# Performance work log

Hardware: AMD Instinct MI355X
Metric: run time of the kernel (lower is better)

## Reference

```python
import jax, jax.numpy as jnp
import numpy as np
from jax import lax

B, C, H, W = 32, 512, 32, 32
NH = 8
ER = 4
DK_RATIO = 0.2
EPS_LN = 1e-6


def _layernorm(t, g, b):
    m = t.mean(-1, keepdims=True)
    v = ((t - m) ** 2).mean(-1, keepdims=True)
    return (t - m) / jnp.sqrt(v + EPS_LN) * g + b


def setup_inputs() -> dict:
    key = jax.random.key(0)
    ks = jax.random.split(key, 24)
    s = 0.02
    dh = C // NH
    return {
        "x": jax.random.normal(ks[0], (B, C, H, W), jnp.float32),
        "mask_u": jax.random.uniform(ks[1], (B, NH, dh, dh), jnp.float32),
        "dw_w": jax.random.normal(ks[2], (C, 1, 3, 3), jnp.float32) * s,
        "dw_b": jnp.zeros((C,), jnp.float32),
        "ln1_g": jnp.ones((C,), jnp.float32),
        "ln1_b": jnp.zeros((C,), jnp.float32),
        "qkv_w": jax.random.normal(ks[3], (3 * C, C), jnp.float32) * s,
        "qkv_b": jnp.zeros((3 * C,), jnp.float32),
        "temp": jnp.ones((NH, 1, 1), jnp.float32),
        "proj_w": jax.random.normal(ks[4], (C, C), jnp.float32) * s,
        "proj_b": jnp.zeros((C,), jnp.float32),
        "ct_w": jax.random.normal(ks[5], (C, C, 2, 2), jnp.float32) * s,  # [in,out,kH,kW]
        "ct_b": jnp.zeros((C,), jnp.float32),
        "ln2_g": jnp.ones((C,), jnp.float32),
        "ln2_b": jnp.zeros((C,), jnp.float32),
        "pw1_w": jax.random.normal(ks[6], (ER * C, C), jnp.float32) * s,
        "pw1_b": jnp.zeros((ER * C,), jnp.float32),
        "pw2_w": jax.random.normal(ks[7], (C, ER * C), jnp.float32) * s,
        "pw2_b": jnp.zeros((C,), jnp.float32),
    }


def reference(x, mask_u, dw_w, dw_b, ln1_g, ln1_b, qkv_w, qkv_b, temp,
              proj_w, proj_b, ct_w, ct_b, ln2_g, ln2_b,
              pw1_w, pw1_b, pw2_w, pw2_b):
    inp = x
    b, c, h, w = x.shape
    # depthwise 3x3 conv + residual
    dw = lax.conv_general_dilated(
        x, dw_w, (1, 1), "SAME", feature_group_count=c,
        dimension_numbers=("NCHW", "OIHW", "NCHW")) + dw_b[None, :, None, None]
    x = dw + inp
    # 2x2 avg pool, stride 2
    hp, wp = h // 2, w // 2
    x = x.reshape(b, c, hp, 2, wp, 2).mean(axis=(3, 5))  # [B,C,hp,wp]
    n = hp * wp
    # tokens [B,N,C] -> LN -> qkv
    t = x.reshape(b, c, n).transpose(0, 2, 1)
    t = _layernorm(t, ln1_g, ln1_b)
    qkv = t @ qkv_w.T + qkv_b                       # [B,N,3C]
    dh = c // NH
    qkv = qkv.reshape(b, n, 3, NH, dh).transpose(2, 0, 3, 1, 4)  # [3,B,h,N,d]
    # cosine (XCA-style) attention: transpose to [B,h,d,N], normalize over N
    q = jnp.swapaxes(qkv[0], -2, -1)
    k = jnp.swapaxes(qkv[1], -2, -1)
    v = jnp.swapaxes(qkv[2], -2, -1)
    q = q / jnp.maximum(jnp.linalg.norm(q, axis=-1, keepdims=True), 1e-12)
    k = k / jnp.maximum(jnp.linalg.norm(k, axis=-1, keepdims=True), 1e-12)
    attn = jnp.einsum("bhdn,bhen->bhde", q, k) * temp  # [B,h,d,d]
    attn = attn + (mask_u < DK_RATIO).astype(attn.dtype) * (-1e12)
    attn = jax.nn.softmax(attn, axis=-1)
    out = jnp.einsum("bhde,bhen->bhdn", attn, v)       # [B,h,d,N]
    out = out.transpose(0, 3, 1, 2).reshape(b, n, c)
    t = out @ proj_w.T + proj_b
    t = t + t
    x = t.transpose(0, 2, 1).reshape(b, c, hp, wp)
    # ConvTranspose2d(C,C,2,stride=2): each pixel expands to 2x2 block
    x = jnp.einsum("bchw,copq->bohpwq", x, ct_w).reshape(b, c, 2 * hp, 2 * wp)
    x = x + ct_b[None, :, None, None]
    # MLP in channels-last
    y = x.transpose(0, 2, 3, 1)                        # [B,H,W,C]
    y = _layernorm(y, ln2_g, ln2_b)
    y = jax.nn.gelu(y @ pw1_w.T + pw1_b, approximate=False)
    y = y @ pw2_w.T + pw2_b
    x = y.transpose(0, 3, 1, 2)
    return inp + x
```

## Files before the change

kernel.cpp:

```cpp
#include <hip/hip_runtime.h>
#include <hip/hip_bf16.h>
#include <math.h>

typedef unsigned short ushort;
typedef __attribute__((ext_vector_type(8))) short short8;
typedef __attribute__((ext_vector_type(8))) unsigned short ushort8;
typedef __attribute__((ext_vector_type(4))) unsigned short ushort4v;
typedef __attribute__((ext_vector_type(4))) float f32x4;

__device__ __forceinline__ ushort f2bb(float v) {
    return __builtin_bit_cast(ushort, __float2bfloat16(v));
}
__device__ __forceinline__ float bf2f(ushort u) {
    return __bfloat162float(__builtin_bit_cast(__hip_bfloat16, u));
}
__device__ __forceinline__ void gl2lds16(const ushort* g, ushort* l) {
    __builtin_amdgcn_global_load_lds(
        (const __attribute__((address_space(1))) unsigned int*)g,
        (__attribute__((address_space(3))) unsigned int*)l, 16, 0, 0);
}


__global__ __launch_bounds__(256) void cvtw_k(const float* __restrict__ in,
                                              ushort* __restrict__ out, int n4) {
    int i = blockIdx.x * 256 + threadIdx.x;
    if (i >= n4) return;
    float4 v = ((const float4*)in)[i];
    ushort4v o;
    o.x = f2bb(v.x); o.y = f2bb(v.y); o.z = f2bb(v.z); o.w = f2bb(v.w);
    ((ushort4v*)out)[i] = o;
}

__global__ __launch_bounds__(256) void cvtt_k(const float* __restrict__ in,
                                              ushort* __restrict__ out) {
    __shared__ float tl[32][33];
    int c0 = blockIdx.y * 32, j0 = blockIdx.x * 32;
    int tr = threadIdx.x >> 5, tc = threadIdx.x & 31;
#pragma unroll
    for (int p4 = 0; p4 < 4; ++p4)
        tl[tr + p4 * 8][tc] = in[(size_t)(c0 + tr + p4 * 8) * 2048 + j0 + tc];
    __syncthreads();
#pragma unroll
    for (int p4 = 0; p4 < 4; ++p4)
        out[(size_t)(j0 + tr + p4 * 8) * 512 + c0 + tc] = f2bb(tl[tc][tr + p4 * 8]);
}

__global__ __launch_bounds__(256) void dwpool_k(const float* __restrict__ x,
                                                const float* __restrict__ dww,
                                                const float* __restrict__ dwb,
                                                ushort* __restrict__ xp) {
    int bc = blockIdx.x;
    int c = bc & 511;
    __shared__ float tile[32][33];
    __shared__ float w9[9];
    const float* xb = x + (size_t)bc * 1024;
    int tid = threadIdx.x;
    for (int i = tid; i < 1024; i += 256) tile[i >> 5][i & 31] = xb[i];
    if (tid < 9) w9[tid] = dww[c * 9 + tid];
    __syncthreads();
    float bv = dwb[c];
    int ph = tid >> 4, pw = tid & 15;
    float s = 0.f;
#pragma unroll
    for (int dy = 0; dy < 2; ++dy) {
#pragma unroll
        for (int dx = 0; dx < 2; ++dx) {
            int hh = 2 * ph + dy, ww = 2 * pw + dx;
            float a = bv + tile[hh][ww];
#pragma unroll
            for (int ky = 0; ky < 3; ++ky) {
                int yy = hh + ky - 1;
                if (yy < 0 || yy > 31) continue;
#pragma unroll
                for (int kx = 0; kx < 3; ++kx) {
                    int xx = ww + kx - 1;
                    if (xx < 0 || xx > 31) continue;
                    a += w9[ky * 3 + kx] * tile[yy][xx];
                }
            }
            s += a;
        }
    }
    xp[(size_t)bc * 256 + tid] = f2bb(0.25f * s);
}

__global__ __launch_bounds__(256) void ln1_stats_k(const ushort* __restrict__ xp,
                                                   float* __restrict__ m1,
                                                   float* __restrict__ r1) {
    __shared__ float sh_s[4][64], sh_q[4][64];
    int blk = blockIdx.x;
    int b = blk >> 2;
    int n0 = (blk & 3) * 64;
    int t = threadIdx.x & 63, w = threadIdx.x >> 6;
    float s = 0.f, ss = 0.f;
    for (int i = 0; i < 128; ++i) {
        int c = w * 128 + i;
        float v = bf2f(xp[(size_t)(b * 512 + c) * 256 + n0 + t]);
        s += v; ss += v * v;
    }
    sh_s[w][t] = s; sh_q[w][t] = ss;
    __syncthreads();
    if (w == 0) {
        s  = sh_s[0][t] + sh_s[1][t] + sh_s[2][t] + sh_s[3][t];
        ss = sh_q[0][t] + sh_q[1][t] + sh_q[2][t] + sh_q[3][t];
        float m = s * (1.0f / 512.0f);
        m1[b * 256 + n0 + t] = m;
        r1[b * 256 + n0 + t] = rsqrtf(ss * (1.0f / 512.0f) - m * m + 1e-6f);
    }
}

__global__ __launch_bounds__(256) void ln1_apply_k(const ushort* __restrict__ xp,
                                                   const float* __restrict__ m1,
                                                   const float* __restrict__ r1,
                                                   const float* __restrict__ g,
                                                   const float* __restrict__ beta,
                                                   ushort* __restrict__ a_ln) {
    __shared__ float tl[64][66];
    int blk = blockIdx.x;
    int b = blk >> 5, ct = (blk >> 2) & 7, nt = blk & 3;
    int t = threadIdx.x;
    int rq = t >> 6, nl = t & 63;
#pragma unroll
    for (int i = 0; i < 16; ++i) {
        int r = rq * 16 + i;
        int c = ct * 64 + r;
        tl[r][nl] = bf2f(xp[(size_t)(b * 512 + c) * 256 + nt * 64 + nl]);
    }
    __syncthreads();
    int r2 = t >> 2, cq = t & 3;
    int m = b * 256 + nt * 64 + r2;
    float mu = m1[m], rs = r1[m];
#pragma unroll
    for (int hh = 0; hh < 2; ++hh) {
        ushort8 o;
#pragma unroll
        for (int j = 0; j < 8; ++j) {
            int cl = cq * 16 + hh * 8 + j;
            int c = ct * 64 + cl;
            o[j] = f2bb((tl[cl][r2] - mu) * rs * g[c] + beta[c]);
        }
        *(ushort8*)&a_ln[(size_t)m * 512 + ct * 64 + cq * 16 + hh * 8] = o;
    }
}

__global__ __launch_bounds__(256) void ln2_fuse_k(ushort* __restrict__ yB,
                                                  ushort* __restrict__ yT,
                                                  const float* __restrict__ g,
                                                  const float* __restrict__ beta) {
    int w = threadIdx.x >> 6, lane = threadIdx.x & 63;
    int row = blockIdx.x * 4 + w;
    ushort* base = (row < 8192) ? (yB + (size_t)row * 512)
                                : (yT + (size_t)(row - 8192) * 512);
    ushort8 raw = *(ushort8*)&base[lane * 8];
    float v[8];
    float s = 0.f, ss = 0.f;
#pragma unroll
    for (int j = 0; j < 8; ++j) { v[j] = bf2f(raw[j]); s += v[j]; ss += v[j] * v[j]; }
#pragma unroll
    for (int off = 1; off < 64; off <<= 1) { s += __shfl_xor(s, off); ss += __shfl_xor(ss, off); }
    float mu = s * (1.0f / 512.0f);
    float rs = rsqrtf(ss * (1.0f / 512.0f) - mu * mu + 1e-6f);
    ushort8 o;
#pragma unroll
    for (int j = 0; j < 8; ++j) {
        int c = lane * 8 + j;
        o[j] = f2bb((v[j] - mu) * rs * g[c] + beta[c]);
    }
    *(ushort8*)&base[lane * 8] = o;
}

struct GP {
    const ushort* A;
    const ushort* W;
    const float* bias;
    ushort* outB;
    ushort* outB2;
    float* outF;
    const float* inp;
    int K, m0;
};

template <int MODE, int BN>
__global__ __launch_bounds__(256) void mgemm_k(GP p) {
    constexpr int MT = (BN == 128) ? 4 : 2;
    constexpr int NT = 4;
    __shared__ ushort As[128 * 32];
    __shared__ ushort Bs[BN * 32];
    int tid = threadIdx.x;
    int lane = tid & 63, w = tid >> 6;
    int lr = lane & 15, lq = lane >> 4;
    int mwoff = (BN == 128) ? (w >> 1) * 64 : w * 32;
    int nwoff = (BN == 128) ? (w & 1) * 64 : 0;
    int gx = gridDim.x;
    int wgid = blockIdx.y * gx + blockIdx.x;
    int cpx = (gx * gridDim.y) >> 3;
    int swz = (wgid & 7) * cpx + (wgid >> 3);
    int bx = swz % gx, by = swz / gx;
    int mbase = by * 128, nbase = bx * BN;
    int lsub = lane >> 2, lcol = (lane & 3) * 8;
    f32x4 acc[MT][NT] = {};

    for (int kb = 0; kb < p.K; kb += 32) {
        __syncthreads();
#pragma unroll
        for (int i = 0; i < 2; ++i) {
            int row = w * 32 + i * 16;
            gl2lds16(p.A + (size_t)(mbase + row + lsub) * p.K + kb + lcol,
                     &As[row * 32]);
        }
        if constexpr (BN == 128) {
#pragma unroll
            for (int i = 0; i < 2; ++i) {
                int row = w * 32 + i * 16;
                gl2lds16(p.W + (size_t)(nbase + row + lsub) * p.K + kb + lcol,
                         &Bs[row * 32]);
            }
        } else {
            int row = w * 16;
            gl2lds16(p.W + (size_t)(nbase + row + lsub) * p.K + kb + lcol,
                     &Bs[row * 32]);
        }
        __syncthreads();
        short8 af[MT], bfr[NT];
#pragma unroll
        for (int t = 0; t < MT; ++t)
            af[t] = *(const short8*)&As[(mwoff + t * 16 + lr) * 32 + lq * 8];
#pragma unroll
        for (int t = 0; t < NT; ++t)
            bfr[t] = *(const short8*)&Bs[(nwoff + t * 16 + lr) * 32 + lq * 8];
#pragma unroll
        for (int i = 0; i < MT; ++i)
#pragma unroll
            for (int j = 0; j < NT; ++j)
                acc[i][j] = __builtin_amdgcn_mfma_f32_16x16x32_bf16(af[i], bfr[j], acc[i][j], 0, 0, 0);
    }

    ushort* ybase = nullptr;
    if constexpr (MODE == 2)
        ybase = (mbase < 2048) ? p.outB : (p.outB2 - (size_t)8192 * 512);
#pragma unroll
    for (int ti = 0; ti < MT; ++ti) {
#pragma unroll
        for (int r = 0; r < 4; ++r) {
            int rg = mbase + mwoff + ti * 16 + lq * 4 + r;
#pragma unroll
            for (int tj = 0; tj < NT; ++tj) {
                int cg = nbase + nwoff + tj * 16 + lr;
                float v = acc[ti][tj][r];
                if constexpr (MODE == 0) {
                    int b = rg >> 8, n = rg & 255;
                    int sect = cg >> 9, h = (cg >> 6) & 7, d = cg & 63;
                    v += p.bias[cg];
                    p.outB[((size_t)(sect * 256 + b * 8 + h) * 64 + d) * 256 + n] = f2bb(v);
                } else if constexpr (MODE == 1) {
                    v = 2.0f * (v + p.bias[cg]);
                    p.outB[(size_t)rg * 512 + cg] = f2bb(v);
                } else if constexpr (MODE == 2) {
                    int o = cg >> 2, pp = (cg >> 1) & 1, qq = cg & 1;
                    int b = rg >> 8, rr = rg & 255, hh = rr >> 4, ww = rr & 15;
                    int pr = (b * 32 + 2 * hh + pp) * 32 + 2 * ww + qq;
                    v += p.bias[o];
                    ybase[(size_t)pr * 512 + o] = f2bb(v);
                } else if constexpr (MODE == 3) {
                    v += p.bias[cg];
                    float ge = 0.5f * v * (1.0f + erff(v * 0.70710678118654752f));
                    p.outB[(size_t)rg * 2048 + cg] = f2bb(ge);
                } else {
                    v += p.bias[cg];
                    int gm = p.m0 + rg;
                    int b = gm >> 10, hw = gm & 1023;
                    size_t idx = ((size_t)(b * 512 + cg)) * 1024 + hw;
                    p.outF[idx] = p.inp[idx] + v;
                }
            }
        }
    }
}

__global__ __launch_bounds__(256) void attn_k(const ushort* __restrict__ qkvp,
                                              const float* __restrict__ mask_u,
                                              const float* __restrict__ temp,
                                              ushort* __restrict__ attn_out) {
    __shared__ float bufA[64 * 65];
    __shared__ float bufB[64 * 65];
    __shared__ float Sb[64 * 65];
    __shared__ float fq[64], fk[64];
    int tid = threadIdx.x;
    int bh = blockIdx.x;
    int b = bh >> 3, h = bh & 7;
    const ushort* q = qkvp + (size_t)bh * 16384;
    const ushort* k = qkvp + 4194304 + (size_t)bh * 16384;
    const ushort* v = qkvp + 8388608 + (size_t)bh * 16384;
    int wv = tid >> 6, lane = tid & 63;

    for (int rr = 0; rr < 16; ++rr) {
        int row = wv * 16 + rr;
        float s = 0.f;
#pragma unroll
        for (int i = 0; i < 4; ++i) { float xv = bf2f(q[row * 256 + lane + i * 64]); s += xv * xv; }
#pragma unroll
        for (int off = 32; off; off >>= 1) s += __shfl_down(s, off);
        if (lane == 0) fq[row] = 1.0f / fmaxf(sqrtf(s), 1e-12f);
        s = 0.f;
#pragma unroll
        for (int i = 0; i < 4; ++i) { float xv = bf2f(k[row * 256 + lane + i * 64]); s += xv * xv; }
#pragma unroll
        for (int off = 32; off; off >>= 1) s += __shfl_down(s, off);
        if (lane == 0) fk[row] = 1.0f / fmaxf(sqrtf(s), 1e-12f);
    }
    __syncthreads();

    int tx = tid & 15, ty = tid >> 4;
    float acc[4][4] = {};
    for (int nb = 0; nb < 256; nb += 64) {
        __syncthreads();
#pragma unroll
        for (int it = 0; it < 16; ++it) {
            int f = it * 256 + tid;
            int d = f >> 6, n = f & 63;
            bufA[d * 65 + n] = bf2f(q[d * 256 + nb + n]);
            bufB[d * 65 + n] = bf2f(k[d * 256 + nb + n]);
        }
        __syncthreads();
#pragma unroll 8
        for (int kk = 0; kk < 64; ++kk) {
            float a[4], bb[4];
#pragma unroll
            for (int i = 0; i < 4; ++i) a[i] = bufA[(ty * 4 + i) * 65 + kk];
#pragma unroll
            for (int j = 0; j < 4; ++j) bb[j] = bufB[(tx * 4 + j) * 65 + kk];
#pragma unroll
            for (int i = 0; i < 4; ++i)
#pragma unroll
                for (int j = 0; j < 4; ++j) acc[i][j] += a[i] * bb[j];
        }
    }
    float tv = temp[h];
    __syncthreads();
#pragma unroll
    for (int i = 0; i < 4; ++i) {
        int d = ty * 4 + i;
#pragma unroll
        for (int j = 0; j < 4; ++j) {
            int e = tx * 4 + j;
            float sc = acc[i][j] * fq[d] * fk[e] * tv;
            float mu = mask_u[((size_t)bh * 64 + d) * 64 + e];
            if (mu < 0.2f) sc -= 1e12f;
            Sb[d * 65 + e] = sc;
        }
    }
    __syncthreads();

    {
        int row = tid >> 2, sub = tid & 3;
        float ev[16];
        float mx = -INFINITY;
#pragma unroll
        for (int i = 0; i < 16; ++i) { float s = Sb[row * 65 + sub * 16 + i]; ev[i] = s; mx = fmaxf(mx, s); }
        mx = fmaxf(mx, __shfl_xor(mx, 1));
        mx = fmaxf(mx, __shfl_xor(mx, 2));
        float sum = 0.f;
#pragma unroll
        for (int i = 0; i < 16; ++i) { ev[i] = expf(ev[i] - mx); sum += ev[i]; }
        sum += __shfl_xor(sum, 1);
        sum += __shfl_xor(sum, 2);
        float inv = 1.0f / sum;
#pragma unroll
        for (int i = 0; i < 16; ++i) Sb[row * 65 + sub * 16 + i] = ev[i] * inv;
    }
    __syncthreads();

    for (int nb = 0; nb < 256; nb += 64) {
        __syncthreads();
#pragma unroll
        for (int it = 0; it < 16; ++it) {
            int f = it * 256 + tid;
            int e = f >> 6, n = f & 63;
            bufA[e * 65 + n] = bf2f(v[e * 256 + nb + n]);
        }
        __syncthreads();
        float o[4][4] = {};
#pragma unroll 8
        for (int kk = 0; kk < 64; ++kk) {
            float a[4], bb[4];
#pragma unroll
            for (int i = 0; i < 4; ++i) a[i] = Sb[(ty * 4 + i) * 65 + kk];
#pragma unroll
            for (int j = 0; j < 4; ++j) bb[j] = bufA[kk * 65 + tx * 4 + j];
#pragma unroll
            for (int i = 0; i < 4; ++i)
#pragma unroll
                for (int j = 0; j < 4; ++j) o[i][j] += a[i] * bb[j];
        }
#pragma unroll
        for (int j = 0; j < 4; ++j) {
            int n = nb + tx * 4 + j;
            size_t base = ((size_t)(b * 256 + n)) * 512 + h * 64 + ty * 4;
#pragma unroll
            for (int i = 0; i < 4; ++i) attn_out[base + i] = f2bb(o[i][j]);
        }
    }
}

extern "C" void kernel_launch(void* const* d_in, const int* in_sizes, int n_in,
                              void* d_out, int out_size, void* d_ws, size_t ws_size,
                              hipStream_t stream) {
    const float* x      = (const float*)d_in[0];
    const float* mask_u = (const float*)d_in[1];
    const float* dw_w   = (const float*)d_in[2];
    const float* dw_b   = (const float*)d_in[3];
    const float* ln1_g  = (const float*)d_in[4];
    const float* ln1_b  = (const float*)d_in[5];
    const float* qkv_w  = (const float*)d_in[6];
    const float* qkv_b  = (const float*)d_in[7];
    const float* temp   = (const float*)d_in[8];
    const float* proj_w = (const float*)d_in[9];
    const float* proj_b = (const float*)d_in[10];
    const float* ct_w   = (const float*)d_in[11];
    const float* ct_b   = (const float*)d_in[12];
    const float* ln2_g  = (const float*)d_in[13];
    const float* ln2_b  = (const float*)d_in[14];
    const float* pw1_w  = (const float*)d_in[15];
    const float* pw1_b  = (const float*)d_in[16];
    const float* pw2_w  = (const float*)d_in[17];
    const float* pw2_b  = (const float*)d_in[18];

    char* wsb = (char*)d_ws;
    float* mean1 = (float*)wsb;
    float* rstd1 = mean1 + 8192;
    float* mean2 = rstd1 + 8192;
    float* rstd2 = mean2 + 32768;
    (void)mean2; (void)rstd2;
    ushort* wq = (ushort*)(wsb + 524288);
    ushort* wp = wq + 786432;
    ushort* wc = wp + 262144;
    ushort* w1 = wc + 1048576;
    ushort* w2 = w1 + 1048576;
    ushort* xp     = (ushort*)(wsb + 8912896);
    ushort* t2     = xp;
    ushort* a_ln   = (ushort*)(wsb + 17301504);
    ushort* yB     = a_ln;
    ushort* qkvp   = (ushort*)(wsb + 25690112);
    ushort* attn_o = (ushort*)(wsb + 50855936);
    ushort* h1c    = qkvp;
    ushort* yT     = (ushort*)(wsb + 59244544);

    cvtw_k<<<768,  256, 0, stream>>>(qkv_w,  wq, 196608);
    cvtw_k<<<256,  256, 0, stream>>>(proj_w, wp, 65536);
    cvtw_k<<<1024, 256, 0, stream>>>(pw1_w,  w1, 262144);
    cvtw_k<<<1024, 256, 0, stream>>>(pw2_w,  w2, 262144);
    cvtt_k<<<dim3(64, 16), 256, 0, stream>>>(ct_w, wc);
    dwpool_k<<<32 * 512, 256, 0, stream>>>(x, dw_w, dw_b, xp);
    ln1_stats_k<<<128, 256, 0, stream>>>(xp, mean1, rstd1);
    ln1_apply_k<<<1024, 256, 0, stream>>>(xp, mean1, rstd1, ln1_g, ln1_b, a_ln);
    {
        GP p{}; p.A = a_ln; p.W = wq; p.bias = qkv_b; p.outB = qkvp; p.K = 512;
        mgemm_k<0, 128><<<dim3(12, 64), 256, 0, stream>>>(p);
    }
    attn_k<<<256, 256, 0, stream>>>(qkvp, mask_u, temp, attn_o);
    {
        GP p{}; p.A = attn_o; p.W = wp; p.bias = proj_b; p.outB = t2; p.K = 512;
        mgemm_k<1, 128><<<dim3(4, 64), 256, 0, stream>>>(p);
    }
    {
        GP p{}; p.A = t2; p.W = wc; p.bias = ct_b;
        p.outB = yB; p.outB2 = yT; p.K = 512;
        mgemm_k<2, 128><<<dim3(16, 64), 256, 0, stream>>>(p);
    }
    ln2_fuse_k<<<8192, 256, 0, stream>>>(yB, yT, ln2_g, ln2_b);
    for (int c = 0; c < 4; ++c) {
        int m0 = c * 8192;
        const ushort* yChunk = (c == 0) ? yB : (yT + (size_t)(m0 - 8192) * 512);
        {
            GP p{}; p.A = yChunk; p.W = w1; p.bias = pw1_b; p.outB = h1c; p.K = 512;
            mgemm_k<3, 128><<<dim3(16, 64), 256, 0, stream>>>(p);
        }
        {
            GP p{}; p.A = h1c; p.W = w2; p.bias = pw2_b;
            p.outF = (float*)d_out; p.inp = x; p.K = 2048; p.m0 = m0;
            mgemm_k<4, 64><<<dim3(8, 64), 256, 0, stream>>>(p);
        }
    }
}
```

Before: 724.3 us.

## Stage GEMM epilogues through LDS for vectorized coalesced stores and swizzle LDS tiles

```diff
diff --git a/kernel.cpp b/kernel.cpp
--- a/kernel.cpp
+++ b/kernel.cpp
@@ -184,8 +184,10 @@
 __global__ __launch_bounds__(256) void mgemm_k(GP p) {
     constexpr int MT = (BN == 128) ? 4 : 2;
     constexpr int NT = 4;
-    __shared__ ushort As[128 * 32];
-    __shared__ ushort Bs[BN * 32];
+    constexpr int SMEM_BYTES = (MODE == 2) ? 20480 : ((MODE == 4) ? 16896 : 16384);
+    __shared__ __align__(16) char smem[SMEM_BYTES];
+    ushort* As = (ushort*)smem;
+    ushort* Bs = As + 128 * 32;
     int tid = threadIdx.x;
     int lane = tid & 63, w = tid >> 6;
     int lr = lane & 15, lq = lane >> 4;
@@ -197,7 +199,10 @@
     int swz = (wgid & 7) * cpx + (wgid >> 3);
     int bx = swz % gx, by = swz / gx;
     int mbase = by * 128, nbase = bx * BN;
-    int lsub = lane >> 2, lcol = (lane & 3) * 8;
+    int lsub = lane >> 2;
+    int cchunk = (lane & 3) ^ ((lsub >> 1) & 3);
+    int lcol = cchunk * 8;
+    int physc = lq ^ ((lr >> 1) & 3);
     f32x4 acc[MT][NT] = {};
 
     for (int kb = 0; kb < p.K; kb += 32) {
@@ -224,10 +229,10 @@
         short8 af[MT], bfr[NT];
 #pragma unroll
         for (int t = 0; t < MT; ++t)
-            af[t] = *(const short8*)&As[(mwoff + t * 16 + lr) * 32 + lq * 8];
+            af[t] = *(const short8*)&As[(mwoff + t * 16 + lr) * 32 + physc * 8];
 #pragma unroll
         for (int t = 0; t < NT; ++t)
-            bfr[t] = *(const short8*)&Bs[(nwoff + t * 16 + lr) * 32 + lq * 8];
+            bfr[t] = *(const short8*)&Bs[(nwoff + t * 16 + lr) * 32 + physc * 8];
 #pragma unroll
         for (int i = 0; i < MT; ++i)
 #pragma unroll
@@ -235,43 +240,136 @@
                 acc[i][j] = __builtin_amdgcn_mfma_f32_16x16x32_bf16(af[i], bfr[j], acc[i][j], 0, 0, 0);
     }
 
-    ushort* ybase = nullptr;
-    if constexpr (MODE == 2)
-        ybase = (mbase < 2048) ? p.outB : (p.outB2 - (size_t)8192 * 512);
-#pragma unroll
-    for (int ti = 0; ti < MT; ++ti) {
-#pragma unroll
-        for (int r = 0; r < 4; ++r) {
-            int rg = mbase + mwoff + ti * 16 + lq * 4 + r;
-#pragma unroll
-            for (int tj = 0; tj < NT; ++tj) {
-                int cg = nbase + nwoff + tj * 16 + lr;
-                float v = acc[ti][tj][r];
-                if constexpr (MODE == 0) {
-                    int b = rg >> 8, n = rg & 255;
-                    int sect = cg >> 9, h = (cg >> 6) & 7, d = cg & 63;
-                    v += p.bias[cg];
-                    p.outB[((size_t)(sect * 256 + b * 8 + h) * 64 + d) * 256 + n] = f2bb(v);
-                } else if constexpr (MODE == 1) {
-                    v = 2.0f * (v + p.bias[cg]);
-                    p.outB[(size_t)rg * 512 + cg] = f2bb(v);
-                } else if constexpr (MODE == 2) {
-                    int o = cg >> 2, pp = (cg >> 1) & 1, qq = cg & 1;
-                    int b = rg >> 8, rr = rg & 255, hh = rr >> 4, ww = rr & 15;
-                    int pr = (b * 32 + 2 * hh + pp) * 32 + 2 * ww + qq;
-                    v += p.bias[o];
-                    ybase[(size_t)pr * 512 + o] = f2bb(v);
-                } else if constexpr (MODE == 3) {
-                    v += p.bias[cg];
-                    float ge = 0.5f * v * (1.0f + erff(v * 0.70710678118654752f));
-                    p.outB[(size_t)rg * 2048 + cg] = f2bb(ge);
-                } else {
-                    v += p.bias[cg];
-                    int gm = p.m0 + rg;
-                    int b = gm >> 10, hw = gm & 1023;
-                    size_t idx = ((size_t)(b * 512 + cg)) * 1024 + hw;
-                    p.outF[idx] = p.inp[idx] + v;
-                }
+    if constexpr (MODE == 1 || MODE == 3) {
+        const size_t LD = (MODE == 1) ? 512 : 2048;
+        ushort* eb = (ushort*)smem;
+#pragma unroll
+        for (int h = 0; h < 2; ++h) {
+            __syncthreads();
+            if ((w & 1) == h) {
+#pragma unroll
+                for (int ti = 0; ti < MT; ++ti)
+#pragma unroll
+                    for (int tj = 0; tj < NT; ++tj)
+#pragma unroll
+                        for (int r = 0; r < 4; ++r) {
+                            int row = mwoff + ti * 16 + lq * 4 + r;
+                            int colh = tj * 16 + lr;
+                            float v = acc[ti][tj][r] + p.bias[nbase + h * 64 + colh];
+                            if constexpr (MODE == 1) v *= 2.0f;
+                            else v = 0.5f * v * (1.0f + erff(v * 0.70710678118654752f));
+                            int ph = (colh >> 3) ^ (row & 7);
+                            eb[row * 64 + ph * 8 + (colh & 7)] = f2bb(v);
+                        }
+            }
+            __syncthreads();
+#pragma unroll
+            for (int i = 0; i < 4; ++i) {
+                int row = i * 32 + (tid >> 3);
+                int ch = tid & 7;
+                int pch = ch ^ (row & 7);
+                short8 d = *(short8*)&eb[row * 64 + pch * 8];
+                *(short8*)&p.outB[(size_t)(mbase + row) * LD + nbase + h * 64 + ch * 8] = d;
+            }
+        }
+    } else if constexpr (MODE == 0) {
+        ushort* eb = (ushort*)smem;
+        int b = mbase >> 8, n0 = mbase & 255;
+#pragma unroll
+        for (int pc = 0; pc < 4; ++pc) {
+            __syncthreads();
+            if ((w & 1) == (pc >> 1)) {
+                int tjb = (pc & 1) * 2;
+#pragma unroll
+                for (int ti = 0; ti < MT; ++ti)
+#pragma unroll
+                    for (int tj2 = 0; tj2 < 2; ++tj2)
+#pragma unroll
+                        for (int r = 0; r < 4; ++r) {
+                            int tj = tjb + tj2;
+                            int row = mwoff + ti * 16 + lq * 4 + r;
+                            int cl = tj2 * 16 + lr;
+                            float v = acc[ti][tj][r] + p.bias[nbase + pc * 32 + cl];
+                            eb[cl * 136 + row] = f2bb(v);
+                        }
+            }
+            __syncthreads();
+#pragma unroll
+            for (int i = 0; i < 2; ++i) {
+                int dl = (tid >> 4) + 16 * i;
+                int ch = tid & 15;
+                short8 d = *(short8*)&eb[dl * 136 + ch * 8];
+                int cg = nbase + pc * 32 + dl;
+                int sect = cg >> 9, hh = (cg >> 6) & 7, dd = cg & 63;
+                size_t addr = ((size_t)(sect * 256 + b * 8 + hh) * 64 + dd) * 256 + n0 + ch * 8;
+                *(short8*)&p.outB[addr] = d;
+            }
+        }
+    } else if constexpr (MODE == 2) {
+        ushort* eb = (ushort*)smem;
+        ushort* ybase = (mbase < 2048) ? p.outB : (p.outB2 - (size_t)8192 * 512);
+        int obase = nbase >> 2;
+#pragma unroll
+        for (int hf = 0; hf < 2; ++hf) {
+            __syncthreads();
+            if ((w >> 1) == hf) {
+#pragma unroll
+                for (int ti = 0; ti < MT; ++ti)
+#pragma unroll
+                    for (int tj = 0; tj < NT; ++tj)
+#pragma unroll
+                        for (int r = 0; r < 4; ++r) {
+                            int rl = (mwoff - hf * 64) + ti * 16 + lq * 4 + r;
+                            int cgl = nwoff + tj * 16 + lr;
+                            int o_l = cgl >> 2, pp = (cgl >> 1) & 1, qq = cgl & 1;
+                            int pix = ((rl >> 4) * 2 + pp) * 32 + (rl & 15) * 2 + qq;
+                            float v = acc[ti][tj][r] + p.bias[obase + o_l];
+                            eb[pix * 40 + o_l] = f2bb(v);
+                        }
+            }
+            __syncthreads();
+            int hhbase = ((mbase & 255) >> 4) + hf * 4;
+            int prb = (mbase >> 8) * 32 + 2 * hhbase;
+#pragma unroll
+            for (int i = 0; i < 4; ++i) {
+                int pix = i * 64 + (tid >> 2);
+                int ch = tid & 3;
+                short8 d = *(short8*)&eb[pix * 40 + ch * 8];
+                int pr = (prb + (pix >> 5)) * 32 + (pix & 31);
+                *(short8*)&ybase[(size_t)pr * 512 + obase + ch * 8] = d;
+            }
+        }
+    } else {
+        float* ef = (float*)smem;
+        int gm0 = p.m0 + mbase;
+        int b = gm0 >> 10, hw0 = gm0 & 1023;
+#pragma unroll
+        for (int pc = 0; pc < 2; ++pc) {
+            __syncthreads();
+#pragma unroll
+            for (int ti = 0; ti < MT; ++ti)
+#pragma unroll
+                for (int tj2 = 0; tj2 < 2; ++tj2)
+#pragma unroll
+                    for (int r = 0; r < 4; ++r) {
+                        int tj = pc * 2 + tj2;
+                        int row = mwoff + ti * 16 + lq * 4 + r;
+                        int cl = tj2 * 16 + lr;
+                        ef[cl * 132 + row] = acc[ti][tj][r] + p.bias[nbase + pc * 32 + cl];
+                    }
+            __syncthreads();
+#pragma unroll
+            for (int i = 0; i < 4; ++i) {
+                int cl = (tid >> 5) + 8 * i;
+                int ck = tid & 31;
+                float4 v4 = *(float4*)&ef[cl * 132 + ck * 4];
+                int c = nbase + pc * 32 + cl;
+                size_t idx = ((size_t)(b * 512 + c)) * 1024 + hw0 + ck * 4;
+                float4 xin = *(const float4*)&p.inp[idx];
+                float4 o4;
+                o4.x = xin.x + v4.x; o4.y = xin.y + v4.y;
+                o4.z = xin.z + v4.z; o4.w = xin.w + v4.w;
+                *(float4*)&p.outF[idx] = o4;
             }
         }
     }
@@ -428,9 +526,6 @@
     char* wsb = (char*)d_ws;
     float* mean1 = (float*)wsb;
     float* rstd1 = mean1 + 8192;
-    float* mean2 = rstd1 + 8192;
-    float* rstd2 = mean2 + 32768;
-    (void)mean2; (void)rstd2;
     ushort* wq = (ushort*)(wsb + 524288);
     ushort* wp = wq + 786432;
     ushort* wc = wp + 262144;
```

Result: no change. 714.9 us (-1.3%).
